# Performance work log

Measured on AMD Instinct MI355X. Metric: run time of the kernel, lower is better.

## Reference

```python
import jax, jax.numpy as jnp
import numpy as np

H, KV, D = 16, 4, 128
EPS = 1e-6

def setup_inputs() -> dict:
    key = jax.random.key(0)
    ks = jax.random.split(key, 7)
    B, S, HS = 2, 2048, 2048
    return {
        "hidden_states": jax.random.normal(ks[0], (B, S, HS), jnp.float32),
        "cos": jax.random.uniform(ks[1], (S, D), jnp.float32),
        "sin": jax.random.uniform(ks[2], (S, D), jnp.float32),
        "Wq": jax.random.normal(ks[3], (H * D, HS), jnp.float32) * 0.02,
        "Wk": jax.random.normal(ks[4], (KV * D, HS), jnp.float32) * 0.02,
        "Wv": jax.random.normal(ks[5], (KV * D, HS), jnp.float32) * 0.02,
        "Wo": jax.random.normal(ks[6], (HS, H * D), jnp.float32) * 0.02,
        "norm_q_w": jnp.ones((D,), jnp.float32),
        "norm_k_w": jnp.ones((D,), jnp.float32),
    }

def _rmsnorm(x, w):
    # RMSNorm over head_dim
    return x * jax.lax.rsqrt(jnp.mean(x * x, axis=-1, keepdims=True) + EPS) * w

def _rope(x, cos, sin):
    # x: [B, S, heads, D]; cos/sin: [S, D]; rotate-half (use_real_unbind_dim=-2)
    c = cos[None, :, None, :]
    s = sin[None, :, None, :]
    x1, x2 = jnp.split(x, 2, axis=-1)
    x_rot = jnp.concatenate([-x2, x1], axis=-1)
    return x * c + x_rot * s

def reference(hidden_states, cos, sin, Wq, Wk, Wv, Wo, norm_q_w, norm_k_w):
    B, S, _ = hidden_states.shape
    q = (hidden_states @ Wq.T).reshape(B, S, H, D)
    k = (hidden_states @ Wk.T).reshape(B, S, KV, D)
    v = (hidden_states @ Wv.T).reshape(B, S, KV, D)
    q = _rmsnorm(q, norm_q_w)
    k = _rmsnorm(k, norm_k_w)
    q = _rope(q, cos, sin)
    k = _rope(k, cos, sin)
    # GQA: repeat_interleave K/V heads to match Q heads
    g = H // KV
    k = jnp.repeat(k, g, axis=2)  # [B, S, H, D]
    v = jnp.repeat(v, g, axis=2)
    scores = jnp.einsum('bqhd,bkhd->bhqk', q, k) * (D ** -0.5)
    attn = jax.nn.softmax(scores, axis=-1)
    out = jnp.einsum('bhqk,bkhd->bqhd', attn, v)  # [B, S, H, D]
    out = out.reshape(B, S, H * D)
    return out @ Wo.T
```

## Files before the change

### kernel.cpp

```cpp
#include <hip/hip_runtime.h>


typedef __attribute__((ext_vector_type(8))) short bf16x8;
typedef __attribute__((ext_vector_type(4))) float f32x4;
typedef __attribute__((ext_vector_type(16))) float f32x16;

__device__ __forceinline__ unsigned short f2bf(float x) {
  union { float f; unsigned u; } v; v.f = x;
  unsigned r = v.u + 0x7fffu + ((v.u >> 16) & 1u);
  return (unsigned short)(r >> 16);
}

__device__ __forceinline__ float bf2f(unsigned short h) {
  union { unsigned u; float f; } v; v.u = (unsigned)h << 16;
  return v.f;
}

__device__ __forceinline__ unsigned cvt_pk_bf16(float lo, float hi) {
  unsigned r;
  asm("v_cvt_pk_bf16_f32 %0, %1, %2" : "=v"(r) : "v"(lo), "v"(hi));
  return r;
}

__device__ __forceinline__ void gload_lds16(const void* g, void* l) {
  __builtin_amdgcn_global_load_lds(
      (const __attribute__((address_space(1))) void*)g,
      (__attribute__((address_space(3))) void*)l, 16, 0, 0);
}

__global__ __launch_bounds__(256) void cvt_all(
    const float4* __restrict__ hs, const float4* __restrict__ wq,
    const float4* __restrict__ wk, const float4* __restrict__ wv,
    const float4* __restrict__ wo, ushort4* __restrict__ X,
    ushort4* __restrict__ Wqkv, ushort4* __restrict__ WoB) {
  int i = blockIdx.x * 256 + threadIdx.x;
  const float4* src;
  ushort4* dst;
  int off;
  if (i < 2097152)      { src = hs; dst = X;               off = 0; }
  else if (i < 3145728) { src = wq; dst = Wqkv;            off = 2097152; }
  else if (i < 3407872) { src = wk; dst = Wqkv + 1048576;  off = 3145728; }
  else if (i < 3670016) { src = wv; dst = Wqkv + 1310720;  off = 3407872; }
  else                  { src = wo; dst = WoB;             off = 3670016; }
  int j = i - off;
  float4 v = src[j];
  dst[j] = make_ushort4(f2bf(v.x), f2bf(v.y), f2bf(v.z), f2bf(v.w));
}

template <int NF, bool OUT_BF16>
__global__ __launch_bounds__(512, 2) void gemm_bt_8ph(
    const unsigned short* __restrict__ A, const unsigned short* __restrict__ Bm,
    void* __restrict__ Cout, int M, int N, int K) {
  __shared__ char lsA[2][32768];
  __shared__ char lsB[2][NF * 8192];
  const int tid = threadIdx.x;
  const int wave = tid >> 6, lane = tid & 63;
  const int lrow = lane & 15, kg = lane >> 4;
  const int wm = wave >> 2, wn = wave & 3;
  const int BN = NF * 64;
  const int nbn = N / BN;
  const int bid = (blockIdx.x & 7) * (gridDim.x >> 3) + (blockIdx.x >> 3);
  const int m0 = (bid / nbn) << 8;
  const int n0 = (bid % nbn) * BN;
  const int NT = K >> 6;

  const int srow = tid >> 2;
  const int scol = (((tid & 3) ^ (srow & 3)) << 3);
  const size_t a0 = (size_t)(m0 + srow) * K + scol;
  const size_t a1 = (size_t)(m0 + 128 + srow) * K + scol;
  const size_t b0 = (size_t)(n0 + srow) * K + scol;
  const size_t b1 = (size_t)(n0 + 128 + srow) * K + scol;

  f32x4 acc[8][NF];
#pragma unroll
  for (int i = 0; i < 8; ++i)
#pragma unroll
    for (int j = 0; j < NF; ++j)
#pragma unroll
      for (int t = 0; t < 4; ++t) acc[i][j][t] = 0.f;

  const int xk = ((kg ^ (lrow & 3)) << 4);
  const int abase = (wm * 128 + lrow) * 64 + xk;
  const int bbase = (wn * NF * 16 + lrow) * 64 + xk;

  auto stage_plane = [&](int T, int ks) {
    if (T >= NT) return;
    const int buf = T & 1;
    const size_t kof = (size_t)T * 64 + ks * 32;
    char* da = lsA[buf] + ks * 16384 + wave * 1024;
    gload_lds16(A + a0 + kof, da);
    gload_lds16(A + a1 + kof, da + 8192);
    char* db = lsB[buf] + ks * (NF * 4096) + wave * 1024;
    gload_lds16(Bm + b0 + kof, db);
    if (NF >= 3) {
      if (tid < 256) gload_lds16(Bm + b1 + kof, db + 8192);
    }
  };

  auto phase = [&](int T, int ks, int sT, int sKs) {
    const int buf = T & 1;
    const char* pa = lsA[buf] + ks * 16384;
    const char* pb = lsB[buf] + ks * (NF * 4096);
    bf16x8 af[8], bfr[NF];
#pragma unroll
    for (int mf = 0; mf < 8; ++mf)
      af[mf] = *(const bf16x8*)(pa + abase + mf * 1024);
#pragma unroll
    for (int nf = 0; nf < NF; ++nf)
      bfr[nf] = *(const bf16x8*)(pb + bbase + nf * 1024);
    stage_plane(sT, sKs);
    asm volatile("s_waitcnt vmcnt(6)" ::: "memory");
    __builtin_amdgcn_s_barrier();
    asm volatile("s_waitcnt lgkmcnt(0)" ::: "memory");
    __builtin_amdgcn_sched_barrier(0);
    __builtin_amdgcn_s_setprio(1);
#pragma unroll
    for (int mf = 0; mf < 8; ++mf)
#pragma unroll
      for (int nf = 0; nf < NF; ++nf)
        acc[mf][nf] =
            __builtin_amdgcn_mfma_f32_16x16x32_bf16(af[mf], bfr[nf], acc[mf][nf], 0, 0, 0);
    __builtin_amdgcn_s_setprio(0);
    __builtin_amdgcn_s_barrier();
  };

  stage_plane(0, 0);
  stage_plane(0, 1);
  stage_plane(1, 0);
  asm volatile("s_waitcnt vmcnt(6)" ::: "memory");
  __builtin_amdgcn_s_barrier();

  for (int kt = 0; kt < NT; ++kt) {
    phase(kt, 0, kt + 1, 1);
    phase(kt, 1, kt + 2, 0);
  }

#pragma unroll
  for (int mf = 0; mf < 8; ++mf) {
#pragma unroll
    for (int nf = 0; nf < NF; ++nf) {
      int row = m0 + wm * 128 + mf * 16 + kg * 4;
      int col = n0 + wn * NF * 16 + nf * 16 + lrow;
      if (OUT_BF16) {
        unsigned short* C = (unsigned short*)Cout;
#pragma unroll
        for (int t = 0; t < 4; ++t)
          C[(size_t)(row + t) * N + col] = f2bf(acc[mf][nf][t]);
      } else {
        float* C = (float*)Cout;
#pragma unroll
        for (int t = 0; t < 4; ++t)
          C[(size_t)(row + t) * N + col] = acc[mf][nf][t];
      }
    }
  }
}

__global__ __launch_bounds__(256) void rms_rope(
    const unsigned short* __restrict__ QKV, const float* __restrict__ cosT,
    const float* __restrict__ sinT, const float* __restrict__ wq,
    const float* __restrict__ wk, unsigned short* __restrict__ Q,
    unsigned short* __restrict__ Kg, unsigned short* __restrict__ Vg) {
  int task = blockIdx.x * 4 + (threadIdx.x >> 6);
  int lane = threadIdx.x & 63;
  int row = task / 24;
  int slot = task - row * 24;
  int b = row >> 11, s = row & 2047;
  const unsigned short* x = QKV + (size_t)row * 3072 + slot * 128;
  float x1 = bf2f(x[lane]), x2 = bf2f(x[lane + 64]);
  if (slot < 20) {
    float ss = x1 * x1 + x2 * x2;
#pragma unroll
    for (int msk = 1; msk < 64; msk <<= 1) ss += __shfl_xor(ss, msk);
    float inv = rsqrtf(ss * (1.0f / 128.0f) + 1e-6f);
    const float* w = (slot < 16) ? wq : wk;
    x1 *= inv * w[lane];
    x2 *= inv * w[lane + 64];
    float c1 = cosT[s * 128 + lane], c2 = cosT[s * 128 + lane + 64];
    float sn1 = sinT[s * 128 + lane], sn2 = sinT[s * 128 + lane + 64];
    float o1 = x1 * c1 - x2 * sn1;
    float o2 = x2 * c2 + x1 * sn2;
    if (slot < 16) {
      const float qs = 0.08838834764831845f * 1.4426950408889634f;
      o1 *= qs; o2 *= qs;
    }
    x1 = o1; x2 = o2;
  }
  if (slot < 16) {
    unsigned short* dst = Q + (((size_t)b * 16 + slot) * 2048 + s) * 128;
    dst[lane] = f2bf(x1);
    dst[lane + 64] = f2bf(x2);
  } else {
    int kv = (slot - 16) & 3;
    size_t tb = ((size_t)((b * 4 + kv) * 32) + (s >> 6)) * 16384;
    int key = s & 63;
    if (slot < 20) {
      char* base = (char*)Kg + tb;
      int kb = (key >> 5) * 512 + (key & 31) * 16;
      int d1 = lane, d2 = lane + 64;
      *(unsigned short*)(base + (d1 >> 4) * 2048 + ((d1 >> 3) & 1) * 1024 + kb + (d1 & 7) * 2) = f2bf(x1);
      *(unsigned short*)(base + (d2 >> 4) * 2048 + ((d2 >> 3) & 1) * 1024 + kb + (d2 & 7) * 2) = f2bf(x2);
    } else {
      char* base = (char*)Vg + tb;
      int p = key >> 4;
      int vhi = (key >> 2) & 1;
      int e = (key & 3) | (((key >> 3) & 1) << 2);
      int off = p * 4096 + vhi * 512 + e * 2;
      int d1 = lane, d2 = lane + 64;
      *(unsigned short*)(base + off + (d1 >> 5) * 1024 + (d1 & 31) * 16) = f2bf(x1);
      *(unsigned short*)(base + off + (d2 >> 5) * 1024 + (d2 & 31) * 16) = f2bf(x2);
    }
  }
}

__global__ __launch_bounds__(256, 3) void attn64(
    const unsigned short* __restrict__ Q, const unsigned short* __restrict__ Kg,
    const unsigned short* __restrict__ Vg, float* __restrict__ P0,
    float* __restrict__ P1, float* __restrict__ Ls) {
  __shared__ unsigned short Kl[2][8192];
  const int tid = threadIdx.x;
  const int wave = tid >> 6, lane = tid & 63;
  const int l31 = lane & 31, hi = lane >> 5;
  int bid = blockIdx.x;
  bid = (bid & 7) * 128 + (bid >> 3);
  const int qt = bid & 15, sp = (bid >> 4) & 1, bh = bid >> 5;
  const int b = bh >> 4, h = bh & 15, kh = h >> 2;
  const char* Kt = (const char*)Kg + (size_t)(b * 4 + kh) * 524288 + (size_t)sp * 262144;
  const char* Vt = (const char*)Vg + (size_t)(b * 4 + kh) * 524288 + (size_t)sp * 262144;
  const unsigned short* Qb =
      Q + ((size_t)(b * 16 + h) * 2048 + qt * 128 + wave * 32) * 128;
  bf16x8 qf[8];
#pragma unroll
  for (int s = 0; s < 8; ++s)
    qf[s] = *(const bf16x8*)(Qb + l31 * 128 + s * 16 + hi * 8);
  f32x16 acc[4];
#pragma unroll
  for (int c = 0; c < 4; ++c)
#pragma unroll
    for (int r = 0; r < 16; ++r) acc[c][r] = 0.f;
  float lsum = 0.f;

  const char* Vlane = Vt + hi * 512 + l31 * 16;
  bf16x8 vr[8];

  auto stageK = [&](int t) {
    const char* kt = Kt + (size_t)t * 16384;
    char* kd = (char*)Kl[t & 1];
#pragma unroll
    for (int c = 0; c < 4; ++c)
      gload_lds16(kt + c * 4096 + tid * 16, kd + c * 4096 + wave * 1024);
  };
  auto loadVh = [&](int t, int h2) {
    const char* vt = Vlane + (size_t)t * 16384 + h2 * 8192;
#pragma unroll
    for (int p = 0; p < 2; ++p)
#pragma unroll
      for (int c = 0; c < 4; ++c)
        vr[p * 4 + c] = *(const bf16x8*)(vt + p * 4096 + c * 1024);
  };

  stageK(0);
  asm volatile("s_waitcnt vmcnt(0)" ::: "memory");
  __builtin_amdgcn_s_barrier();

  f32x16 s0, s1;
  for (int t = 0; t < 16; ++t) {
    if (t < 15) stageK(t + 1);
    {
      const char* Kb = (const char*)Kl[t & 1] + hi * 1024 + l31 * 16;
#pragma unroll
      for (int r = 0; r < 16; ++r) { s0[r] = 0.f; s1[r] = 0.f; }
      __builtin_amdgcn_s_setprio(1);
#pragma unroll
      for (int s = 0; s < 8; ++s) {
        bf16x8 k0 = *(const bf16x8*)(Kb + s * 2048);
        bf16x8 k1 = *(const bf16x8*)(Kb + s * 2048 + 512);
        s0 = __builtin_amdgcn_mfma_f32_32x32x16_bf16(k0, qf[s], s0, 0, 0, 0);
        s1 = __builtin_amdgcn_mfma_f32_32x32x16_bf16(k1, qf[s], s1, 0, 0, 0);
      }
      __builtin_amdgcn_s_setprio(0);
    }
    float p0[16], p1[16];
#pragma unroll
    for (int r = 0; r < 16; ++r) {
      p0[r] = exp2f(s0[r]);
      p1[r] = exp2f(s1[r]);
    }
    float u8[8];
#pragma unroll
    for (int r = 0; r < 8; ++r) u8[r] = (p0[r] + p0[r + 8]) + (p1[r] + p1[r + 8]);
#pragma unroll
    for (int r = 0; r < 4; ++r) u8[r] += u8[r + 4];
    lsum += (u8[0] + u8[1]) + (u8[2] + u8[3]);
    union { bf16x8 v[4]; unsigned w[16]; } pa;
#pragma unroll
    for (int r = 0; r < 4; ++r) {
      pa.w[r]      = cvt_pk_bf16(p0[2 * r], p0[2 * r + 1]);
      pa.w[4 + r]  = cvt_pk_bf16(p0[8 + 2 * r], p0[9 + 2 * r]);
      pa.w[8 + r]  = cvt_pk_bf16(p1[2 * r], p1[2 * r + 1]);
      pa.w[12 + r] = cvt_pk_bf16(p1[8 + 2 * r], p1[9 + 2 * r]);
    }
    loadVh(t, 0);
    __builtin_amdgcn_sched_barrier(0);
    __builtin_amdgcn_s_setprio(1);
#pragma unroll
    for (int p = 0; p < 2; ++p)
#pragma unroll
      for (int c = 0; c < 4; ++c)
        acc[c] = __builtin_amdgcn_mfma_f32_32x32x16_bf16(pa.v[p], vr[p * 4 + c], acc[c], 0, 0, 0);
    __builtin_amdgcn_s_setprio(0);
    __builtin_amdgcn_sched_barrier(0);
    loadVh(t, 1);
    __builtin_amdgcn_sched_barrier(0);
    __builtin_amdgcn_s_setprio(1);
#pragma unroll
    for (int p = 0; p < 2; ++p)
#pragma unroll
      for (int c = 0; c < 4; ++c)
        acc[c] = __builtin_amdgcn_mfma_f32_32x32x16_bf16(pa.v[2 + p], vr[p * 4 + c], acc[c], 0, 0, 0);
    __builtin_amdgcn_s_setprio(0);
    if (t < 15) {
      asm volatile("s_waitcnt vmcnt(0)" ::: "memory");
      __builtin_amdgcn_s_barrier();
    }
  }

  lsum += __shfl_xor(lsum, 32);
  float* Pp = sp ? P1 : P0;
  if (hi == 0) {
    int srow = qt * 128 + wave * 32 + l31;
    Ls[(size_t)sp * 65536 + ((size_t)b * 2048 + srow) * 16 + h] = lsum;
  }
#pragma unroll
  for (int r = 0; r < 16; ++r) {
    int q = (r & 3) + 8 * (r >> 2) + 4 * hi;
    int srow = qt * 128 + wave * 32 + q;
    float* dst = Pp + (((size_t)b * 2048 + srow) * 16 + h) * 128;
#pragma unroll
    for (int c = 0; c < 4; ++c)
      dst[c * 32 + l31] = acc[c][r];
  }
}

__global__ __launch_bounds__(256) void attn_combine(
    const float* __restrict__ P0, const float* __restrict__ P1,
    const float* __restrict__ Ls, unsigned short* __restrict__ Ob) {
  int gid = blockIdx.x * 256 + threadIdx.x;
  int row = gid >> 4, c = gid & 15;
  float inv = 1.0f / (Ls[row] + Ls[65536 + row]);
  const float4* a = (const float4*)(P0 + (size_t)row * 128 + c * 8);
  const float4* bb = (const float4*)(P1 + (size_t)row * 128 + c * 8);
  float4 a0 = a[0], a1 = a[1], b0 = bb[0], b1 = bb[1];
  union { bf16x8 v; unsigned short u[8]; } o;
  o.u[0] = f2bf((a0.x + b0.x) * inv);
  o.u[1] = f2bf((a0.y + b0.y) * inv);
  o.u[2] = f2bf((a0.z + b0.z) * inv);
  o.u[3] = f2bf((a0.w + b0.w) * inv);
  o.u[4] = f2bf((a1.x + b1.x) * inv);
  o.u[5] = f2bf((a1.y + b1.y) * inv);
  o.u[6] = f2bf((a1.z + b1.z) * inv);
  o.u[7] = f2bf((a1.w + b1.w) * inv);
  *(bf16x8*)(Ob + (size_t)row * 128 + c * 8) = o.v;
}

extern "C" void kernel_launch(void* const* d_in, const int* in_sizes, int n_in,
                              void* d_out, int out_size, void* d_ws, size_t ws_size,
                              hipStream_t stream) {
  const float* hs   = (const float*)d_in[0];
  const float* cosT = (const float*)d_in[1];
  const float* sinT = (const float*)d_in[2];
  const float* Wq   = (const float*)d_in[3];
  const float* Wk   = (const float*)d_in[4];
  const float* Wv   = (const float*)d_in[5];
  const float* Wo   = (const float*)d_in[6];
  const float* nqw  = (const float*)d_in[7];
  const float* nkw  = (const float*)d_in[8];
  float* out = (float*)d_out;

  char* ws = (char*)d_ws;
  unsigned short* WoB  = (unsigned short*)ws;
  unsigned short* Qb   = WoB + 4194304;
  unsigned short* Kg   = Qb + 8388608;
  unsigned short* Vg   = Kg + 2097152;
  unsigned short* X    = Vg + 2097152;
  unsigned short* Wqkv = X + 8388608;
  unsigned short* QKVb = Wqkv + 6291456;
  float* P0            = (float*)X;
  float* P1            = P0 + 8388608;
  float* Ls            = P1 + 8388608;
  unsigned short* Ob   = Qb;

  cvt_all<<<18432, 256, 0, stream>>>((const float4*)hs, (const float4*)Wq,
                                     (const float4*)Wk, (const float4*)Wv,
                                     (const float4*)Wo, (ushort4*)X,
                                     (ushort4*)Wqkv, (ushort4*)WoB);

  gemm_bt_8ph<3, true><<<256, 512, 0, stream>>>(X, Wqkv, QKVb, 4096, 3072, 2048);

  rms_rope<<<24576, 256, 0, stream>>>(QKVb, cosT, sinT, nqw, nkw, Qb, Kg, Vg);

  attn64<<<1024, 256, 0, stream>>>(Qb, Kg, Vg, P0, P1, Ls);

  attn_combine<<<4096, 256, 0, stream>>>(P0, P1, Ls, Ob);

  gemm_bt_8ph<2, false><<<256, 512, 0, stream>>>(Ob, WoB, out, 4096, 2048, 2048);
}
```

Baseline: 240.6 us.

## Shrink attention key tiles to 32 and split KV range unevenly

Changes the packed K/V layout from 64-key tiles to 32-key tiles and makes the attention loop step 32 keys at a time with half-size LDS buffers. V register loads for the next tile are now issued at the end of the current iteration, with a partial vmcnt wait, so they overlap the barrier. The key range is split 43/21 tiles between the two split passes instead of evenly, and block indexing changes to match. Smaller tiles cut LDS use and registers but double the loop iterations and barriers. The uneven split only balances if the consumer of P0/P1 and the launch grid agree with it.

New measurement: 250.4 us. 1.04x slower.

```diff
diff --git a/kernel.cpp b/kernel.cpp
--- a/kernel.cpp
+++ b/kernel.cpp
@@ -192,20 +192,18 @@
     dst[lane + 64] = f2bf(x2);
   } else {
     int kv = (slot - 16) & 3;
-    size_t tb = ((size_t)((b * 4 + kv) * 32) + (s >> 6)) * 16384;
-    int key = s & 63;
+    size_t tb = ((size_t)((b * 4 + kv) * 64) + (s >> 5)) * 8192;
+    int key = s & 31;
     if (slot < 20) {
       char* base = (char*)Kg + tb;
-      int kb = (key >> 5) * 512 + (key & 31) * 16;
+      int kb = key * 16;
       int d1 = lane, d2 = lane + 64;
-      *(unsigned short*)(base + (d1 >> 4) * 2048 + ((d1 >> 3) & 1) * 1024 + kb + (d1 & 7) * 2) = f2bf(x1);
-      *(unsigned short*)(base + (d2 >> 4) * 2048 + ((d2 >> 3) & 1) * 1024 + kb + (d2 & 7) * 2) = f2bf(x2);
+      *(unsigned short*)(base + (d1 >> 4) * 1024 + ((d1 >> 3) & 1) * 512 + kb + (d1 & 7) * 2) = f2bf(x1);
+      *(unsigned short*)(base + (d2 >> 4) * 1024 + ((d2 >> 3) & 1) * 512 + kb + (d2 & 7) * 2) = f2bf(x2);
     } else {
       char* base = (char*)Vg + tb;
-      int p = key >> 4;
-      int vhi = (key >> 2) & 1;
-      int e = (key & 3) | (((key >> 3) & 1) << 2);
-      int off = p * 4096 + vhi * 512 + e * 2;
+      int off = (key >> 4) * 4096 + ((key >> 2) & 1) * 512 +
+                ((key & 3) | (((key >> 3) & 1) << 2)) * 2;
       int d1 = lane, d2 = lane + 64;
       *(unsigned short*)(base + off + (d1 >> 5) * 1024 + (d1 & 31) * 16) = f2bf(x1);
       *(unsigned short*)(base + off + (d2 >> 5) * 1024 + (d2 & 31) * 16) = f2bf(x2);
@@ -217,16 +215,20 @@
     const unsigned short* __restrict__ Q, const unsigned short* __restrict__ Kg,
     const unsigned short* __restrict__ Vg, float* __restrict__ P0,
     float* __restrict__ P1, float* __restrict__ Ls) {
-  __shared__ unsigned short Kl[2][8192];
+  __shared__ unsigned short Kl[2][4096];
   const int tid = threadIdx.x;
   const int wave = tid >> 6, lane = tid & 63;
   const int l31 = lane & 31, hi = lane >> 5;
-  int bid = blockIdx.x;
-  bid = (bid & 7) * 128 + (bid >> 3);
-  const int qt = bid & 15, sp = (bid >> 4) & 1, bh = bid >> 5;
+  const int raw = blockIdx.x;
+  const int sp = raw >> 9;
+  const int within = raw & 511;
+  const int id = (within & 7) * 64 + (within >> 3);
+  const int bh = id >> 4, qt = id & 15;
   const int b = bh >> 4, h = bh & 15, kh = h >> 2;
-  const char* Kt = (const char*)Kg + (size_t)(b * 4 + kh) * 524288 + (size_t)sp * 262144;
-  const char* Vt = (const char*)Vg + (size_t)(b * 4 + kh) * 524288 + (size_t)sp * 262144;
+  const int t0 = sp ? 43 : 0;
+  const int t1 = sp ? 64 : 43;
+  const char* Kt = (const char*)Kg + (size_t)(b * 4 + kh) * 524288;
+  const char* Vt = (const char*)Vg + (size_t)(b * 4 + kh) * 524288;
   const unsigned short* Qb =
       Q + ((size_t)(b * 16 + h) * 2048 + qt * 128 + wave * 32) * 128;
   bf16x8 qf[8];
@@ -244,14 +246,13 @@
   bf16x8 vr[8];
 
   auto stageK = [&](int t) {
-    const char* kt = Kt + (size_t)t * 16384;
+    const char* kt = Kt + (size_t)t * 8192;
     char* kd = (char*)Kl[t & 1];
-#pragma unroll
-    for (int c = 0; c < 4; ++c)
-      gload_lds16(kt + c * 4096 + tid * 16, kd + c * 4096 + wave * 1024);
+    gload_lds16(kt + tid * 16, kd + wave * 1024);
+    gload_lds16(kt + 4096 + tid * 16, kd + 4096 + wave * 1024);
   };
-  auto loadVh = [&](int t, int h2) {
-    const char* vt = Vlane + (size_t)t * 16384 + h2 * 8192;
+  auto loadV = [&](int t) {
+    const char* vt = Vlane + (size_t)t * 8192;
 #pragma unroll
     for (int p = 0; p < 2; ++p)
 #pragma unroll
@@ -259,49 +260,39 @@
         vr[p * 4 + c] = *(const bf16x8*)(vt + p * 4096 + c * 1024);
   };
 
-  stageK(0);
+  stageK(t0);
+  loadV(t0);
   asm volatile("s_waitcnt vmcnt(0)" ::: "memory");
   __builtin_amdgcn_s_barrier();
 
-  f32x16 s0, s1;
-  for (int t = 0; t < 16; ++t) {
-    if (t < 15) stageK(t + 1);
+  f32x16 s0;
+  for (int t = t0; t < t1; ++t) {
+    if (t + 1 < t1) stageK(t + 1);
     {
-      const char* Kb = (const char*)Kl[t & 1] + hi * 1024 + l31 * 16;
-#pragma unroll
-      for (int r = 0; r < 16; ++r) { s0[r] = 0.f; s1[r] = 0.f; }
+      const char* Kb = (const char*)Kl[t & 1] + hi * 512 + l31 * 16;
+#pragma unroll
+      for (int r = 0; r < 16; ++r) s0[r] = 0.f;
       __builtin_amdgcn_s_setprio(1);
 #pragma unroll
       for (int s = 0; s < 8; ++s) {
-        bf16x8 k0 = *(const bf16x8*)(Kb + s * 2048);
-        bf16x8 k1 = *(const bf16x8*)(Kb + s * 2048 + 512);
+        bf16x8 k0 = *(const bf16x8*)(Kb + s * 1024);
         s0 = __builtin_amdgcn_mfma_f32_32x32x16_bf16(k0, qf[s], s0, 0, 0, 0);
-        s1 = __builtin_amdgcn_mfma_f32_32x32x16_bf16(k1, qf[s], s1, 0, 0, 0);
       }
       __builtin_amdgcn_s_setprio(0);
     }
-    float p0[16], p1[16];
-#pragma unroll
-    for (int r = 0; r < 16; ++r) {
-      p0[r] = exp2f(s0[r]);
-      p1[r] = exp2f(s1[r]);
-    }
-    float u8[8];
-#pragma unroll
-    for (int r = 0; r < 8; ++r) u8[r] = (p0[r] + p0[r + 8]) + (p1[r] + p1[r + 8]);
-#pragma unroll
-    for (int r = 0; r < 4; ++r) u8[r] += u8[r + 4];
-    lsum += (u8[0] + u8[1]) + (u8[2] + u8[3]);
-    union { bf16x8 v[4]; unsigned w[16]; } pa;
+    float p0[16];
+#pragma unroll
+    for (int r = 0; r < 16; ++r) p0[r] = exp2f(s0[r]);
+    float u4[4];
+#pragma unroll
+    for (int r = 0; r < 4; ++r) u4[r] = (p0[r] + p0[r + 4]) + (p0[r + 8] + p0[r + 12]);
+    lsum += (u4[0] + u4[1]) + (u4[2] + u4[3]);
+    union { bf16x8 v[2]; unsigned w[8]; } pa;
 #pragma unroll
     for (int r = 0; r < 4; ++r) {
-      pa.w[r]      = cvt_pk_bf16(p0[2 * r], p0[2 * r + 1]);
-      pa.w[4 + r]  = cvt_pk_bf16(p0[8 + 2 * r], p0[9 + 2 * r]);
-      pa.w[8 + r]  = cvt_pk_bf16(p1[2 * r], p1[2 * r + 1]);
-      pa.w[12 + r] = cvt_pk_bf16(p1[8 + 2 * r], p1[9 + 2 * r]);
-    }
-    loadVh(t, 0);
-    __builtin_amdgcn_sched_barrier(0);
+      pa.w[r]     = cvt_pk_bf16(p0[2 * r], p0[2 * r + 1]);
+      pa.w[4 + r] = cvt_pk_bf16(p0[8 + 2 * r], p0[9 + 2 * r]);
+    }
     __builtin_amdgcn_s_setprio(1);
 #pragma unroll
     for (int p = 0; p < 2; ++p)
@@ -309,18 +300,9 @@
       for (int c = 0; c < 4; ++c)
         acc[c] = __builtin_amdgcn_mfma_f32_32x32x16_bf16(pa.v[p], vr[p * 4 + c], acc[c], 0, 0, 0);
     __builtin_amdgcn_s_setprio(0);
-    __builtin_amdgcn_sched_barrier(0);
-    loadVh(t, 1);
-    __builtin_amdgcn_sched_barrier(0);
-    __builtin_amdgcn_s_setprio(1);
-#pragma unroll
-    for (int p = 0; p < 2; ++p)
-#pragma unroll
-      for (int c = 0; c < 4; ++c)
-        acc[c] = __builtin_amdgcn_mfma_f32_32x32x16_bf16(pa.v[2 + p], vr[p * 4 + c], acc[c], 0, 0, 0);
-    __builtin_amdgcn_s_setprio(0);
-    if (t < 15) {
-      asm volatile("s_waitcnt vmcnt(0)" ::: "memory");
+    if (t + 1 < t1) {
+      loadV(t + 1);
+      asm volatile("s_waitcnt vmcnt(8)" ::: "memory");
       __builtin_amdgcn_s_barrier();
     }
   }
```
